# Performance work log

Measured on AMD Instinct MI355X. Metric: run time of the kernel, lower is better.

The kernel has to match this reference:

```python
import jax, jax.numpy as jnp
import numpy as np

N_AGT = 65536
N_CTX = 65536
E = 400000
D_AGT = 128
D_CTX = 128
EPS = 1e-5


def gn(x, w, b):
    # GroupNorm with num_groups=1 over channel dim of [N, C]
    m = jnp.mean(x, axis=-1, keepdims=True)
    v = jnp.mean((x - m) ** 2, axis=-1, keepdims=True)
    return (x - m) * jax.lax.rsqrt(v + EPS) * w + b


def setup_inputs() -> dict:
    key = jax.random.key(0)
    ks = jax.random.split(key, 24)
    s = 0.05
    inp = {
        "agts": jax.random.normal(ks[0], (N_AGT, D_AGT), jnp.float32),
        "ctx": jax.random.normal(ks[1], (N_CTX, D_CTX), jnp.float32),
        "agt_ctrs": jax.random.normal(ks[2], (N_AGT, 2), jnp.float32),
        "ctx_ctrs": jax.random.normal(ks[3], (N_CTX, 2), jnp.float32),
        "hi": jax.random.randint(ks[4], (E,), 0, N_AGT),
        "wi": jax.random.randint(ks[5], (E,), 0, N_CTX),
        # dist: Linear(2, n_ctx) + bias, ReLU, Linear(n_ctx, n_ctx) GN ng=1
        "dist_w1": jax.random.normal(ks[6], (2, D_CTX), jnp.float32) * s,
        "dist_b1": jnp.zeros((D_CTX,), jnp.float32),
        "dist_w2": jax.random.normal(ks[7], (D_CTX, D_CTX), jnp.float32) * s,
        "dist_gw": jnp.ones((D_CTX,), jnp.float32),
        "dist_gb": jnp.zeros((D_CTX,), jnp.float32),
        # query: Linear(n_agt, n_ctx) GN ng=1
        "q_w": jax.random.normal(ks[8], (D_AGT, D_CTX), jnp.float32) * s,
        "q_gw": jnp.ones((D_CTX,), jnp.float32),
        "q_gb": jnp.zeros((D_CTX,), jnp.float32),
        # ctx: Linear(3*n_ctx, n_agt) GN, then Linear(n_agt, n_agt, bias=False)
        "ctx_w1": jax.random.normal(ks[9], (3 * D_CTX, D_AGT), jnp.float32) * s,
        "ctx_gw": jnp.ones((D_AGT,), jnp.float32),
        "ctx_gb": jnp.zeros((D_AGT,), jnp.float32),
        "ctx_w2": jax.random.normal(ks[10], (D_AGT, D_AGT), jnp.float32) * s,
        # agt: Linear(n_agt, n_agt, bias=False)
        "agt_w": jax.random.normal(ks[11], (D_AGT, D_AGT), jnp.float32) * s,
        # norm: GroupNorm(1, n_agt)
        "norm_w": jnp.ones((D_AGT,), jnp.float32),
        "norm_b": jnp.zeros((D_AGT,), jnp.float32),
        # linear: Linear(n_agt, n_agt) GN, act=False
        "lin_w": jax.random.normal(ks[12], (D_AGT, D_AGT), jnp.float32) * s,
        "lin_gw": jnp.ones((D_AGT,), jnp.float32),
        "lin_gb": jnp.zeros((D_AGT,), jnp.float32),
    }
    return inp


def reference(agts, ctx, agt_ctrs, ctx_ctrs, hi, wi,
              dist_w1, dist_b1, dist_w2, dist_gw, dist_gb,
              q_w, q_gw, q_gb,
              ctx_w1, ctx_gw, ctx_gb, ctx_w2,
              agt_w, norm_w, norm_b,
              lin_w, lin_gw, lin_gb):
    res = agts
    # edge features: relative displacement -> dist MLP
    d = agt_ctrs[hi] - ctx_ctrs[wi]                      # [E, 2]
    d = jax.nn.relu(d @ dist_w1 + dist_b1)               # [E, D_CTX]
    d = jax.nn.relu(gn(d @ dist_w2, dist_gw, dist_gb))
    # query from gathered agent features
    q = jax.nn.relu(gn(agts[hi] @ q_w, q_gw, q_gb))      # [E, D_CTX]
    # gathered context features
    c = ctx[wi]                                          # [E, D_CTX]
    m = jnp.concatenate([d, q, c], axis=1)               # [E, 3*D_CTX]
    m = jax.nn.relu(gn(m @ ctx_w1, ctx_gw, ctx_gb))      # [E, D_AGT]
    m = m @ ctx_w2                                       # [E, D_AGT]
    # aggregate messages back to agents (scatter-add)
    out = agts @ agt_w
    out = out.at[hi].add(m)
    out = jax.nn.relu(gn(out, norm_w, norm_b))
    out = gn(out @ lin_w, lin_gw, lin_gb)                # act=False
    out = jax.nn.relu(out + res)
    return out
```

## Files before the change

kernel.cpp:

```cpp
#include <hip/hip_runtime.h>
#include <hip/hip_bf16.h>

#define TILE_E 32
#define WSTRIDE 132
#define SB 136
#define SF 132
#define FS 16384

#define FRAG_DW2 0
#define FRAG_W1D 1
#define FRAG_CW2 2
#define FRAG_AGT 3
#define FRAG_QW  4
#define FRAG_W1Q 5
#define FRAG_W1C 6
#define FRAG_LIN 7

typedef __attribute__((ext_vector_type(8))) short short8;
typedef __attribute__((ext_vector_type(4))) float f32x4;

__device__ __forceinline__ unsigned short f2bf(float f) {
    union { float f; unsigned u; } v; v.f = f;
    unsigned r = v.u + 0x7fff + ((v.u >> 16) & 1);
    return (unsigned short)(r >> 16);
}

__device__ __forceinline__ float bf2f(unsigned short u) {
    union { unsigned v; float f; } x; x.v = ((unsigned)u) << 16; return x.f;
}

__device__ __forceinline__ f32x4 mfma16(short8 a, short8 b, f32x4 c) {
    return __builtin_amdgcn_mfma_f32_16x16x32_bf16(a, b, c, 0, 0, 0);
}

__device__ __forceinline__ void load_bfrags_fast(const unsigned short* __restrict__ F,
                                                 int wv, int lane, short8 wB[2][4])
{
#pragma unroll
    for (int cb = 0; cb < 2; ++cb)
#pragma unroll
    for (int kc = 0; kc < 4; ++kc)
        wB[cb][kc] = *(const short8*)(F + ((((wv * 2 + cb) * 4 + kc) * 64 + lane) << 3));
}

__device__ __forceinline__ void mfma_gemm32(const unsigned short* __restrict__ X,
                                            const short8 wB[2][4],
                                            f32x4 acc[2][2], int lane)
{
    const int r  = lane & 15;
    const int kg = (lane >> 4) & 3;
#pragma unroll
    for (int rb = 0; rb < 2; ++rb) {
        const unsigned short* xp = X + (rb * 16 + r) * SB + kg * 8;
#pragma unroll
        for (int kc = 0; kc < 4; ++kc) {
            short8 a = *(const short8*)(xp + kc * 32);
            acc[rb][0] = mfma16(a, wB[0][kc], acc[rb][0]);
            acc[rb][1] = mfma16(a, wB[1][kc], acc[rb][1]);
        }
    }
}

__device__ __forceinline__ void gn_core_pack(float vals[16],
                                             const float* __restrict__ gw,
                                             const float* __restrict__ gb,
                                             int c0, short8& o0, short8& o1)
{
    float s1 = 0.f, s2 = 0.f;
#pragma unroll
    for (int i = 0; i < 16; ++i) { s1 += vals[i]; s2 += vals[i] * vals[i]; }
#pragma unroll
    for (int off = 4; off >= 1; off >>= 1) {
        s1 += __shfl_xor(s1, off);
        s2 += __shfl_xor(s2, off);
    }
    float m   = s1 * (1.f / 128.f);
    float var = fmaxf(s2 * (1.f / 128.f) - m * m, 0.f);
    float isc = rsqrtf(var + 1e-5f);
#pragma unroll
    for (int i = 0; i < 16; ++i) {
        float y = fmaxf((vals[i] - m) * isc * gw[c0 + i] + gb[c0 + i], 0.f);
        unsigned short u = f2bf(y);
        if (i < 8) o0[i] = (short)u; else o1[i - 8] = (short)u;
    }
}

__device__ __forceinline__ void gn_row_to_bf16(const float* __restrict__ sY,
                                               const float* __restrict__ gw,
                                               const float* __restrict__ gb,
                                               unsigned short* __restrict__ dst,
                                               int r8, int c0)
{
    const float4* yv = (const float4*)(sY + r8 * SF + c0);
    float4 a = yv[0], b = yv[1], c = yv[2], d = yv[3];
    float vals[16] = { a.x,a.y,a.z,a.w, b.x,b.y,b.z,b.w,
                       c.x,c.y,c.z,c.w, d.x,d.y,d.z,d.w };
    short8 o0, o1;
    gn_core_pack(vals, gw, gb, c0, o0, o1);
    short8* dp = (short8*)(dst + r8 * SB + c0);
    dp[0] = o0; dp[1] = o1;
}

__device__ __forceinline__ void gn_bf_to_bf16(const unsigned short* __restrict__ sYb,
                                              const float* __restrict__ gw,
                                              const float* __restrict__ gb,
                                              unsigned short* __restrict__ dst,
                                              int r8, int c0)
{
    const short8* yv = (const short8*)(sYb + r8 * SB + c0);
    short8 a = yv[0], b = yv[1];
    float vals[16];
#pragma unroll
    for (int i = 0; i < 8; ++i) {
        vals[i]     = bf2f((unsigned short)a[i]);
        vals[8 + i] = bf2f((unsigned short)b[i]);
    }
    short8 o0, o1;
    gn_core_pack(vals, gw, gb, c0, o0, o1);
    short8* dp = (short8*)(dst + r8 * SB + c0);
    dp[0] = o0; dp[1] = o1;
}

__global__ __launch_bounds__(256) void prep_hist_kernel(
    const float* __restrict__ W0, const float* __restrict__ W1,
    const float* __restrict__ W2, const float* __restrict__ W3,
    const float* __restrict__ W4, const float* __restrict__ W5,
    const float* __restrict__ W6, const float* __restrict__ W7,
    unsigned short* __restrict__ dst,
    const int* __restrict__ hi, int* __restrict__ hist, int E)
{
    const int b = blockIdx.x;
    if (b < 512) {
        int t = b * 256 + threadIdx.x;
        int m = t >> 14;
        int e = t & (FS - 1);
        int j    = e & 7;
        int lane = (e >> 3) & 63;
        int kc   = (e >> 9) & 3;
        int cb   = (e >> 11) & 1;
        int wv   = (e >> 12) & 3;
        int k = kc * 32 + ((lane >> 4) & 3) * 8 + j;
        int c = wv * 32 + cb * 16 + (lane & 15);
        const float* W = m == 0 ? W0 : m == 1 ? W1 : m == 2 ? W2 : m == 3 ? W3
                       : m == 4 ? W4 : m == 5 ? W5 : m == 6 ? W6 : W7;
        dst[t] = f2bf(W[k * 128 + c]);
    } else {
        for (int i = (b - 512) * 256 + threadIdx.x; i < E; i += 256 * 256)
            atomicAdd(&hist[hi[i]], 1);
    }
}

__global__ __launch_bounds__(256) void scanA_kernel(const int* __restrict__ hist,
                                                    int* __restrict__ csum, int nbins)
{
    __shared__ int red[4];
    int b = blockIdx.x;
    int idx = b * 256 + threadIdx.x;
    int v = (idx < nbins) ? hist[idx] : 0;
#pragma unroll
    for (int off = 32; off >= 1; off >>= 1) v += __shfl_xor(v, off);
    if ((threadIdx.x & 63) == 0) red[threadIdx.x >> 6] = v;
    __syncthreads();
    if (threadIdx.x == 0) csum[b] = red[0] + red[1] + red[2] + red[3];
}

__global__ __launch_bounds__(256) void scanBC_kernel(const int* __restrict__ hist,
                                                     const int* __restrict__ csum,
                                                     int* __restrict__ binCtr,
                                                     int nbins, int nchunks)
{
    __shared__ int part[256];
    __shared__ int red[4];
    __shared__ int coffb;
    const int b = blockIdx.x, t = threadIdx.x;

    int cv = (t < b && t < nchunks) ? csum[t] : 0;
#pragma unroll
    for (int off = 32; off >= 1; off >>= 1) cv += __shfl_xor(cv, off);
    if ((t & 63) == 0) red[t >> 6] = cv;
    __syncthreads();
    if (t == 0) coffb = red[0] + red[1] + red[2] + red[3];

    int idx = b * 256 + t;
    int v = (idx < nbins) ? hist[idx] : 0;
    part[t] = v;
    __syncthreads();
    for (int off = 1; off < 256; off <<= 1) {
        int p = (t >= off) ? part[t - off] : 0;
        __syncthreads();
        part[t] += p;
        __syncthreads();
    }
    if (idx < nbins) binCtr[idx] = part[t] - v + coffb;
}

__device__ __forceinline__ void kq_tile_body(
    int tile, const float* __restrict__ agts,
    const float* __restrict__ q_gw, const float* __restrict__ q_gb,
    const unsigned short* __restrict__ frags,
    float* __restrict__ qm, int N,
    unsigned short* sX, float* sY, float* sGw, float* sGb)
{
    const int tid  = threadIdx.x;
    const int lane = tid & 63;
    const int wv   = tid >> 6;
    const int colbase = wv * 32;
    const int r8 = tid >> 3, c0 = (tid & 7) * 16;
    const int cl = lane & 15, rq = lane >> 4;

    short8 wBq[2][4], wB1[2][4];
    load_bfrags_fast(frags + FRAG_QW  * FS, wv, lane, wBq);
    load_bfrags_fast(frags + FRAG_W1Q * FS, wv, lane, wB1);
    if (tid < 128) { sGw[tid] = q_gw[tid]; sGb[tid] = q_gb[tid]; }

    const int base = tile * 32;
    {
        int row = base + r8; if (row >= N) row = N - 1;
        const float* src = agts + (size_t)row * 128 + c0;
        short8 v0, v1;
#pragma unroll
        for (int i = 0; i < 8; ++i) { v0[i] = (short)f2bf(src[i]); v1[i] = (short)f2bf(src[i + 8]); }
        short8* dp = (short8*)(sX + r8 * SB + c0);
        dp[0] = v0; dp[1] = v1;
    }
    __syncthreads();

    f32x4 aQ[2][2] = {{{0,0,0,0},{0,0,0,0}},{{0,0,0,0},{0,0,0,0}}};
    mfma_gemm32(sX, wBq, aQ, lane);
    {
#pragma unroll
        for (int rb = 0; rb < 2; ++rb)
#pragma unroll
        for (int cb = 0; cb < 2; ++cb)
#pragma unroll
        for (int q = 0; q < 4; ++q)
            sY[(rb * 16 + rq * 4 + q) * SF + colbase + cb * 16 + cl] = aQ[rb][cb][q];
    }
    __syncthreads();
    gn_row_to_bf16(sY, sGw, sGb, sX, r8, c0);
    __syncthreads();

    f32x4 aM[2][2] = {{{0,0,0,0},{0,0,0,0}},{{0,0,0,0},{0,0,0,0}}};
    mfma_gemm32(sX, wB1, aM, lane);
#pragma unroll
    for (int rb = 0; rb < 2; ++rb)
#pragma unroll
    for (int q = 0; q < 4; ++q) {
        int row = base + rb * 16 + rq * 4 + q;
        if (row < N) {
            float2 v = make_float2(aM[rb][0][q], aM[rb][1][q]);
            *(float2*)(qm + (size_t)row * 128 + colbase + cl * 2) = v;
        }
    }
}

__device__ __forceinline__ void kc_tile_body(
    int tile, const float* __restrict__ ctx,
    const unsigned short* __restrict__ frags,
    float* __restrict__ cm, int N, unsigned short* sX)
{
    const int tid  = threadIdx.x;
    const int lane = tid & 63;
    const int wv   = tid >> 6;
    const int colbase = wv * 32;
    const int r8 = tid >> 3, c0 = (tid & 7) * 16;
    const int cl = lane & 15, rq = lane >> 4;

    short8 wB[2][4];
    load_bfrags_fast(frags + FRAG_W1C * FS, wv, lane, wB);

    const int base = tile * 32;
    {
        int row = base + r8; if (row >= N) row = N - 1;
        const float* src = ctx + (size_t)row * 128 + c0;
        short8 v0, v1;
#pragma unroll
        for (int i = 0; i < 8; ++i) { v0[i] = (short)f2bf(src[i]); v1[i] = (short)f2bf(src[i + 8]); }
        short8* dp = (short8*)(sX + r8 * SB + c0);
        dp[0] = v0; dp[1] = v1;
    }
    __syncthreads();

    f32x4 acc[2][2] = {{{0,0,0,0},{0,0,0,0}},{{0,0,0,0},{0,0,0,0}}};
    mfma_gemm32(sX, wB, acc, lane);
#pragma unroll
    for (int rb = 0; rb < 2; ++rb)
#pragma unroll
    for (int q = 0; q < 4; ++q) {
        int row = base + rb * 16 + rq * 4 + q;
        if (row < N) {
            float2 v = make_float2(acc[rb][0][q], acc[rb][1][q]);
            *(float2*)(cm + (size_t)row * 128 + colbase + cl * 2) = v;
        }
    }
}

__global__ __launch_bounds__(256) void nodes_kernel(
    const int* __restrict__ hi, const int* __restrict__ wi,
    const float* __restrict__ agt_ctrs, const float* __restrict__ ctx_ctrs,
    int* __restrict__ binCtr,
    int* __restrict__ hiS, int* __restrict__ wiS,
    float* __restrict__ dxS, float* __restrict__ dyS,
    const float* __restrict__ agts, const float* __restrict__ ctx,
    const float* __restrict__ q_gw, const float* __restrict__ q_gb,
    const unsigned short* __restrict__ frags,
    float* __restrict__ qm, float* __restrict__ cm,
    int E, int N, int NC, int tilesA)
{
    __shared__ __align__(16) unsigned short sX[32 * SB];
    __shared__ __align__(16) float sY[32 * SF];
    __shared__ float sGw[128], sGb[128];

    const int b = blockIdx.x;
    if (b < 256) {
        for (int i = b * 256 + threadIdx.x; i < E; i += 256 * 256) {
            int h = hi[i], w = wi[i];
            int p = atomicAdd(&binCtr[h], 1);
            hiS[p] = h; wiS[p] = w;
            dxS[p] = agt_ctrs[2 * h]     - ctx_ctrs[2 * w];
            dyS[p] = agt_ctrs[2 * h + 1] - ctx_ctrs[2 * w + 1];
        }
        return;
    }
    int t = b - 256;
    if (t < tilesA)
        kq_tile_body(t, agts, q_gw, q_gb, frags, qm, N, sX, sY, sGw, sGb);
    else
        kc_tile_body(t - tilesA, ctx, frags, cm, NC, sX);
}

__global__ __launch_bounds__(256, 3) void edge_sorted_kernel(
    const int* __restrict__ hiS, const int* __restrict__ wiS,
    const float* __restrict__ dxS, const float* __restrict__ dyS,
    const float* __restrict__ dist_w1, const float* __restrict__ dist_b1,
    const float* __restrict__ dist_gw, const float* __restrict__ dist_gb,
    const float* __restrict__ ctx_gw, const float* __restrict__ ctx_gb,
    const unsigned short* __restrict__ frags,
    const float* __restrict__ qm, const float* __restrict__ cm,
    float* __restrict__ msum, int E, int numTiles)
{
    __shared__ __align__(16) unsigned short sH[32 * SB];
    __shared__ __align__(16) unsigned short sYb[32 * SB];
    __shared__ float sW1[3][128];
    __shared__ float sDGw[128], sDGb[128], sCGw[128], sCGb[128];
    __shared__ int sHiA[32], sWiA[32], sKey[33];
    __shared__ float sDx[32], sDy[32];

    const int tid  = threadIdx.x;
    const int lane = tid & 63;
    const int wv   = tid >> 6;
    const int colbase = wv * 32;
    const int r8 = tid >> 3, c0 = (tid & 7) * 16;
    const int cl = lane & 15, rq = lane >> 4;

    short8 wBh[2][4], wBd[2][4];
    load_bfrags_fast(frags + FRAG_DW2 * FS, wv, lane, wBh);
    load_bfrags_fast(frags + FRAG_W1D * FS, wv, lane, wBd);
    if (tid < 128) {
        sW1[0][tid] = dist_w1[tid];
        sW1[1][tid] = dist_w1[128 + tid];
        sW1[2][tid] = dist_b1[tid];
        sDGw[tid] = dist_gw[tid]; sDGb[tid] = dist_gb[tid];
        sCGw[tid] = ctx_gw[tid];  sCGb[tid] = ctx_gb[tid];
    }

    int ph = 0, pw = 0, pkey = -1; float pdx = 0.f, pdy = 0.f;
    if (tid < 32) {
        pkey = -1 - tid;
        int e = blockIdx.x * 32 + tid;
        if (e < E) { ph = hiS[e]; pw = wiS[e]; pkey = ph; pdx = dxS[e]; pdy = dyS[e]; }
    }

    for (int tile = blockIdx.x; tile < numTiles; tile += gridDim.x) {
        __syncthreads();
        if (tid < 32) {
            sHiA[tid] = ph; sWiA[tid] = pw; sKey[tid] = pkey;
            sDx[tid] = pdx; sDy[tid] = pdy;
        }
        __syncthreads();

        if (tid < 32) {
            pkey = -1 - tid; ph = 0; pw = 0; pdx = 0.f; pdy = 0.f;
            int tn = tile + gridDim.x;
            if (tn < numTiles) {
                int e = tn * 32 + tid;
                if (e < E) { ph = hiS[e]; pw = wiS[e]; pkey = ph; pdx = dxS[e]; pdy = dyS[e]; }
            }
        }

        float2 gq[2][4], gc[2][4];
#pragma unroll
        for (int rb = 0; rb < 2; ++rb)
#pragma unroll
        for (int q = 0; q < 4; ++q) {
            int r = rb * 16 + rq * 4 + q;
            gq[rb][q] = *(const float2*)(qm + (size_t)sHiA[r] * 128 + colbase + cl * 2);
            gc[rb][q] = *(const float2*)(cm + (size_t)sWiA[r] * 128 + colbase + cl * 2);
        }

        {
            float dx = sDx[r8], dy = sDy[r8];
            short8 o0, o1;
#pragma unroll
            for (int i = 0; i < 16; ++i) {
                int c = c0 + i;
                float v = fmaf(dx, sW1[0][c], fmaf(dy, sW1[1][c], sW1[2][c]));
                unsigned short u = f2bf(fmaxf(v, 0.f));
                if (i < 8) o0[i] = (short)u; else o1[i - 8] = (short)u;
            }
            short8* dp = (short8*)(sH + r8 * SB + c0);
            dp[0] = o0; dp[1] = o1;
        }
        __syncthreads();

        f32x4 acc[2][2] = {{{0,0,0,0},{0,0,0,0}},{{0,0,0,0},{0,0,0,0}}};
        mfma_gemm32(sH, wBh, acc, lane);
        {
#pragma unroll
            for (int rb = 0; rb < 2; ++rb)
#pragma unroll
            for (int cb = 0; cb < 2; ++cb)
#pragma unroll
            for (int q = 0; q < 4; ++q)
                sYb[(rb * 16 + rq * 4 + q) * SB + colbase + cb * 16 + cl] = f2bf(acc[rb][cb][q]);
        }
        __syncthreads();
        gn_bf_to_bf16(sYb, sDGw, sDGb, sH, r8, c0);
        __syncthreads();

        f32x4 a2[2][2];
#pragma unroll
        for (int rb = 0; rb < 2; ++rb)
#pragma unroll
        for (int q = 0; q < 4; ++q) {
            a2[rb][0][q] = gq[rb][q].x + gc[rb][q].x;
            a2[rb][1][q] = gq[rb][q].y + gc[rb][q].y;
        }
        mfma_gemm32(sH, wBd, a2, lane);
        {
#pragma unroll
            for (int rb = 0; rb < 2; ++rb)
#pragma unroll
            for (int cb = 0; cb < 2; ++cb)
#pragma unroll
            for (int q = 0; q < 4; ++q)
                sYb[(rb * 16 + rq * 4 + q) * SB + colbase + cb * 16 + cl] = f2bf(a2[rb][cb][q]);
        }
        __syncthreads();
        gn_bf_to_bf16(sYb, sCGw, sCGb, sH, r8, c0);
        __syncthreads();

        {
            const int col   = tid & 127;
            const int rbase = (tid >> 7) * 16;
            float sum = 0.f;
#pragma unroll
            for (int i = 0; i < 16; ++i) {
                int r = rbase + i;
                sum += bf2f(sH[r * SB + col]);
                bool segEnd = (i == 15) || (sKey[r + 1] != sKey[r]);
                if (segEnd) {
                    int key = sKey[r];
                    if (key >= 0) atomicAdd(&msum[(size_t)key * 128 + col], sum);
                    sum = 0.f;
                }
            }
        }
    }
}

__global__ __launch_bounds__(256) void final_mfma_kernel(
    const float* __restrict__ agts, const float* __restrict__ msum,
    const float* __restrict__ norm_w, const float* __restrict__ norm_b,
    const float* __restrict__ lin_gw, const float* __restrict__ lin_gb,
    const unsigned short* __restrict__ frags,
    float* __restrict__ out, int N)
{
    __shared__ __align__(16) unsigned short sXa[32 * SB];
    __shared__ __align__(16) unsigned short sXm[32 * SB];
    __shared__ float sNw[128], sNb[128], sLw[128], sLb[128];

    const int tid  = threadIdx.x;
    const int lane = tid & 63;
    const int wv   = tid >> 6;
    const int colbase = wv * 32;
    const int r8 = tid >> 3, c0 = (tid & 7) * 16;
    const int cl = lane & 15, rq = lane >> 4;

    short8 wBa[2][4], wB2[2][4], wBl[2][4];
    load_bfrags_fast(frags + FRAG_AGT * FS, wv, lane, wBa);
    load_bfrags_fast(frags + FRAG_CW2 * FS, wv, lane, wB2);
    load_bfrags_fast(frags + FRAG_LIN * FS, wv, lane, wBl);
    if (tid < 128) {
        sNw[tid] = norm_w[tid]; sNb[tid] = norm_b[tid];
        sLw[tid] = lin_gw[tid]; sLb[tid] = lin_gb[tid];
    }

    const int base = blockIdx.x * 32;
    {
        int row = base + r8; if (row >= N) row = N - 1;
        const float* sa = agts + (size_t)row * 128 + c0;
        const float* sm = msum + (size_t)row * 128 + c0;
        short8 a0, a1, m0, m1;
#pragma unroll
        for (int i = 0; i < 8; ++i) {
            a0[i] = (short)f2bf(sa[i]); a1[i] = (short)f2bf(sa[i + 8]);
            m0[i] = (short)f2bf(sm[i]); m1[i] = (short)f2bf(sm[i + 8]);
        }
        short8* da = (short8*)(sXa + r8 * SB + c0);
        short8* dm = (short8*)(sXm + r8 * SB + c0);
        da[0] = a0; da[1] = a1; dm[0] = m0; dm[1] = m1;
    }
    __syncthreads();

    f32x4 acc[2][2] = {{{0,0,0,0},{0,0,0,0}},{{0,0,0,0},{0,0,0,0}}};
    mfma_gemm32(sXa, wBa, acc, lane);
    mfma_gemm32(sXm, wB2, acc, lane);
    __syncthreads();
    {
#pragma unroll
        for (int rb = 0; rb < 2; ++rb)
#pragma unroll
        for (int cb = 0; cb < 2; ++cb)
#pragma unroll
        for (int q = 0; q < 4; ++q)
            sXm[(rb * 16 + rq * 4 + q) * SB + colbase + cb * 16 + cl] = f2bf(acc[rb][cb][q]);
    }
    __syncthreads();
    gn_bf_to_bf16(sXm, sNw, sNb, sXa, r8, c0);
    __syncthreads();

    f32x4 aL[2][2] = {{{0,0,0,0},{0,0,0,0}},{{0,0,0,0},{0,0,0,0}}};
    mfma_gemm32(sXa, wBl, aL, lane);
    __syncthreads();
    {
#pragma unroll
        for (int rb = 0; rb < 2; ++rb)
#pragma unroll
        for (int cb = 0; cb < 2; ++cb)
#pragma unroll
        for (int q = 0; q < 4; ++q)
            sXm[(rb * 16 + rq * 4 + q) * SB + colbase + cb * 16 + cl] = f2bf(aL[rb][cb][q]);
    }
    __syncthreads();
    {
        int row = base + r8;
        if (row < N) {
            const short8* yv = (const short8*)(sXm + r8 * SB + c0);
            short8 a = yv[0], b = yv[1];
            float vals[16]; float s1 = 0.f, s2 = 0.f;
#pragma unroll
            for (int i = 0; i < 8; ++i) {
                vals[i]     = bf2f((unsigned short)a[i]);
                vals[8 + i] = bf2f((unsigned short)b[i]);
            }
#pragma unroll
            for (int i = 0; i < 16; ++i) { s1 += vals[i]; s2 += vals[i] * vals[i]; }
#pragma unroll
            for (int off = 4; off >= 1; off >>= 1) {
                s1 += __shfl_xor(s1, off);
                s2 += __shfl_xor(s2, off);
            }
            float m   = s1 * (1.f / 128.f);
            float var = fmaxf(s2 * (1.f / 128.f) - m * m, 0.f);
            float isc = rsqrtf(var + 1e-5f);
            const float* rp = agts + (size_t)row * 128 + c0;
            float* op = out + (size_t)row * 128 + c0;
#pragma unroll
            for (int i = 0; i < 16; ++i) {
                float y = (vals[i] - m) * isc * sLw[c0 + i] + sLb[c0 + i] + rp[i];
                op[i] = fmaxf(y, 0.f);
            }
        }
    }
}

__device__ __forceinline__ void gemm_tile(const float* __restrict__ sX,
                                          const float* __restrict__ sWT,
                                          int lc, int rg,
                                          float acc0[8], float acc1[8])
{
    const float* w0p = sWT + lc * WSTRIDE;
    const float* w1p = sWT + (lc + 64) * WSTRIDE;
    const float* xp  = sX + rg * 8 * WSTRIDE;
#pragma unroll 4
    for (int k = 0; k < 128; k += 4) {
        float4 w0 = *(const float4*)(w0p + k);
        float4 w1 = *(const float4*)(w1p + k);
#pragma unroll
        for (int j = 0; j < 8; ++j) {
            float4 x = *(const float4*)(xp + j * WSTRIDE + k);
            acc0[j] = fmaf(x.x, w0.x, acc0[j]);
            acc0[j] = fmaf(x.y, w0.y, acc0[j]);
            acc0[j] = fmaf(x.z, w0.z, acc0[j]);
            acc0[j] = fmaf(x.w, w0.w, acc0[j]);
            acc1[j] = fmaf(x.x, w1.x, acc1[j]);
            acc1[j] = fmaf(x.y, w1.y, acc1[j]);
            acc1[j] = fmaf(x.z, w1.z, acc1[j]);
            acc1[j] = fmaf(x.w, w1.w, acc1[j]);
        }
    }
}

__device__ __forceinline__ void stage_wt(const float* __restrict__ W,
                                         float* __restrict__ sWT, int tid)
{
    const int c  = tid & 127;
    const int k0 = tid >> 7;
    float*       dst = sWT + c * WSTRIDE + k0;
    const float* src = W + tid;
    float v[16];
#pragma unroll
    for (int p = 0; p < 4; ++p) {
#pragma unroll
        for (int i = 0; i < 16; ++i) v[i] = src[(p * 16 + i) * 256];
#pragma unroll
        for (int i = 0; i < 16; ++i) dst[(p * 16 + i) * 2] = v[i];
    }
}

__device__ __forceinline__ void gn_rows_lds(const float acc0[8], const float acc1[8],
                                            float gw0, float gw1, float gb0, float gb1,
                                            bool relu, float* __restrict__ dst,
                                            int lc, int rg)
{
#pragma unroll
    for (int j = 0; j < 8; ++j) {
        float s1 = acc0[j] + acc1[j];
        float s2 = acc0[j] * acc0[j] + acc1[j] * acc1[j];
#pragma unroll
        for (int off = 32; off >= 1; off >>= 1) {
            s1 += __shfl_xor(s1, off);
            s2 += __shfl_xor(s2, off);
        }
        float m   = s1 * (1.f / 128.f);
        float var = fmaxf(s2 * (1.f / 128.f) - m * m, 0.f);
        float isc = rsqrtf(var + 1e-5f);
        float y0  = (acc0[j] - m) * isc * gw0 + gb0;
        float y1  = (acc1[j] - m) * isc * gw1 + gb1;
        if (relu) { y0 = fmaxf(y0, 0.f); y1 = fmaxf(y1, 0.f); }
        int r = rg * 8 + j;
        dst[r * WSTRIDE + lc]      = y0;
        dst[r * WSTRIDE + lc + 64] = y1;
    }
}

__global__ __launch_bounds__(256) void rowgemm_kernel(
    const float* __restrict__ X, const float* __restrict__ W,
    float* __restrict__ Y, int n)
{
    __shared__ float sWT[128 * WSTRIDE];
    __shared__ float sX[TILE_E * WSTRIDE];
    const int tid  = threadIdx.x;
    const int base = blockIdx.x * TILE_E;
    {
        int r = tid >> 3, c0 = (tid & 7) * 16;
        int row = base + r;
        if (row < n) {
            const float* src = X + (size_t)row * 128 + c0;
            float*       dst = sX + r * WSTRIDE + c0;
#pragma unroll
            for (int i = 0; i < 4; ++i)
                *(float4*)(dst + i * 4) = *(const float4*)(src + i * 4);
        }
    }
    stage_wt(W, sWT, tid);
    __syncthreads();
    const int lc = tid & 63, rg = tid >> 6;
    float acc0[8] = {0,0,0,0,0,0,0,0}, acc1[8] = {0,0,0,0,0,0,0,0};
    gemm_tile(sX, sWT, lc, rg, acc0, acc1);
#pragma unroll
    for (int j = 0; j < 8; ++j) {
        int row = base + rg * 8 + j;
        if (row < n) {
            Y[(size_t)row * 128 + lc]      = acc0[j];
            Y[(size_t)row * 128 + lc + 64] = acc1[j];
        }
    }
}

__global__ __launch_bounds__(256) void edge_kernel(
    const float* __restrict__ agt_ctrs, const float* __restrict__ ctx_ctrs,
    const int* __restrict__ hi, const int* __restrict__ wi,
    const float* __restrict__ qsrc, const float* __restrict__ ctx,
    const float* __restrict__ dist_w1, const float* __restrict__ dist_b1,
    const float* __restrict__ dist_w2,
    const float* __restrict__ dist_gw, const float* __restrict__ dist_gb,
    const float* __restrict__ q_w,
    const float* __restrict__ q_gw, const float* __restrict__ q_gb,
    const float* __restrict__ ctx_w1,
    const float* __restrict__ ctx_gw, const float* __restrict__ ctx_gb,
    const float* __restrict__ ctx_w2,
    float* __restrict__ out, int E, int numTiles)
{
    __shared__ float sWT[128 * WSTRIDE];
    __shared__ float sH2[TILE_E * WSTRIDE];
    __shared__ float sD2[TILE_E * WSTRIDE];
    __shared__ float sQ2[TILE_E * WSTRIDE];
    __shared__ float sC2[TILE_E * WSTRIDE];
    __shared__ int   sHi[TILE_E];
    __shared__ int   sWiB[TILE_E];
    __shared__ float sDx2[TILE_E], sDy2[TILE_E];

    const int tid = threadIdx.x;
    const int lc = tid & 63, rg = tid >> 6;

    const float dgw0 = dist_gw[lc], dgw1 = dist_gw[lc + 64];
    const float dgb0 = dist_gb[lc], dgb1 = dist_gb[lc + 64];
    const float cgw0 = ctx_gw[lc],  cgw1 = ctx_gw[lc + 64];
    const float cgb0 = ctx_gb[lc],  cgb1 = ctx_gb[lc + 64];
    const float qgw0 = q_gw[lc], qgw1 = q_gw[lc + 64];
    const float qgb0 = q_gb[lc], qgb1 = q_gb[lc + 64];
    const int   hc  = tid & 127;
    const int   hrg = tid >> 7;
    const float w1x = dist_w1[hc], w1y = dist_w1[128 + hc], b1c = dist_b1[hc];

    for (int tile = blockIdx.x; tile < numTiles; tile += gridDim.x) {
        const int base = tile * TILE_E;
        __syncthreads();
        if (tid < TILE_E) {
            int e = base + tid;
            int h = 0, w = 0;
            if (e < E) { h = hi[e]; w = wi[e]; }
            sHi[tid]  = h;
            sWiB[tid] = w;
            sDx2[tid] = agt_ctrs[2 * h]     - ctx_ctrs[2 * w];
            sDy2[tid] = agt_ctrs[2 * h + 1] - ctx_ctrs[2 * w + 1];
        }
        __syncthreads();
        {
            int r = tid >> 3, c0 = (tid & 7) * 16;
            int h = sHi[r], w = sWiB[r];
            const float* qs = qsrc + (size_t)h * 128 + c0;
            const float* cs = ctx  + (size_t)w * 128 + c0;
            float* qd = sQ2 + r * WSTRIDE + c0;
            float* cd = sC2 + r * WSTRIDE + c0;
#pragma unroll
            for (int i = 0; i < 4; ++i) {
                *(float4*)(qd + i * 4) = *(const float4*)(qs + i * 4);
                *(float4*)(cd + i * 4) = *(const float4*)(cs + i * 4);
            }
        }
        {
#pragma unroll
            for (int j = 0; j < 16; ++j) {
                int r = hrg * 16 + j;
                float v = fmaf(sDx2[r], w1x, fmaf(sDy2[r], w1y, b1c));
                sH2[r * WSTRIDE + hc] = fmaxf(v, 0.f);
            }
        }
        __syncthreads();
        stage_wt(q_w, sWT, tid);
        __syncthreads();
        {
            float a0[8] = {0,0,0,0,0,0,0,0}, a1[8] = {0,0,0,0,0,0,0,0};
            gemm_tile(sQ2, sWT, lc, rg, a0, a1);
            __syncthreads();
            gn_rows_lds(a0, a1, qgw0, qgw1, qgb0, qgb1, true, sQ2, lc, rg);
        }
        __syncthreads();
        stage_wt(dist_w2, sWT, tid);
        __syncthreads();
        {
            float a0[8] = {0,0,0,0,0,0,0,0}, a1[8] = {0,0,0,0,0,0,0,0};
            gemm_tile(sH2, sWT, lc, rg, a0, a1);
            gn_rows_lds(a0, a1, dgw0, dgw1, dgb0, dgb1, true, sD2, lc, rg);
        }
        float m0[8] = {0,0,0,0,0,0,0,0}, m1[8] = {0,0,0,0,0,0,0,0};
        __syncthreads();
        stage_wt(ctx_w1, sWT, tid);
        __syncthreads();
        gemm_tile(sD2, sWT, lc, rg, m0, m1);
        __syncthreads();
        stage_wt(ctx_w1 + 128 * 128, sWT, tid);
        __syncthreads();
        gemm_tile(sQ2, sWT, lc, rg, m0, m1);
        __syncthreads();
        stage_wt(ctx_w1 + 2 * 128 * 128, sWT, tid);
        __syncthreads();
        gemm_tile(sC2, sWT, lc, rg, m0, m1);
        gn_rows_lds(m0, m1, cgw0, cgw1, cgb0, cgb1, true, sH2, lc, rg);
        __syncthreads();
        stage_wt(ctx_w2, sWT, tid);
        __syncthreads();
        {
            float a0[8] = {0,0,0,0,0,0,0,0}, a1[8] = {0,0,0,0,0,0,0,0};
            gemm_tile(sH2, sWT, lc, rg, a0, a1);
#pragma unroll
            for (int j = 0; j < 8; ++j) {
                int r = rg * 8 + j;
                int e = base + r;
                if (e < E) {
                    int h = sHi[r];
                    atomicAdd(&out[(size_t)h * 128 + lc],      a0[j]);
                    atomicAdd(&out[(size_t)h * 128 + lc + 64], a1[j]);
                }
            }
        }
    }
}

__global__ __launch_bounds__(256) void final_kernel(
    const float* __restrict__ agts,
    const float* __restrict__ norm_w, const float* __restrict__ norm_b,
    const float* __restrict__ lin_w,
    const float* __restrict__ lin_gw, const float* __restrict__ lin_gb,
    float* __restrict__ out, int n)
{
    __shared__ float sWT[128 * WSTRIDE];
    __shared__ float sX[TILE_E * WSTRIDE];
    const int tid  = threadIdx.x;
    const int base = blockIdx.x * TILE_E;
    {
        int r = tid >> 3, c0 = (tid & 7) * 16;
        int row = base + r;
        if (row < n) {
            const float* src = out + (size_t)row * 128 + c0;
            float vals[16];
            float s1 = 0.f, s2 = 0.f;
#pragma unroll
            for (int i = 0; i < 16; ++i) {
                float v = src[i];
                vals[i] = v; s1 += v; s2 += v * v;
            }
#pragma unroll
            for (int off = 4; off >= 1; off >>= 1) {
                s1 += __shfl_xor(s1, off);
                s2 += __shfl_xor(s2, off);
            }
            float m   = s1 * (1.f / 128.f);
            float var = fmaxf(s2 * (1.f / 128.f) - m * m, 0.f);
            float isc = rsqrtf(var + 1e-5f);
            float* dst = sX + r * WSTRIDE + c0;
#pragma unroll
            for (int i = 0; i < 16; ++i) {
                int c = c0 + i;
                float y = (vals[i] - m) * isc * norm_w[c] + norm_b[c];
                dst[i] = fmaxf(y, 0.f);
            }
        }
    }
    stage_wt(lin_w, sWT, tid);
    __syncthreads();
    const int lc = tid & 63, rg = tid >> 6;
    float acc0[8] = {0,0,0,0,0,0,0,0}, acc1[8] = {0,0,0,0,0,0,0,0};
    gemm_tile(sX, sWT, lc, rg, acc0, acc1);
    const float lgw0 = lin_gw[lc], lgw1 = lin_gw[lc + 64];
    const float lgb0 = lin_gb[lc], lgb1 = lin_gb[lc + 64];
#pragma unroll
    for (int j = 0; j < 8; ++j) {
        float s1 = acc0[j] + acc1[j];
        float s2 = acc0[j] * acc0[j] + acc1[j] * acc1[j];
#pragma unroll
        for (int off = 32; off >= 1; off >>= 1) {
            s1 += __shfl_xor(s1, off);
            s2 += __shfl_xor(s2, off);
        }
        float m   = s1 * (1.f / 128.f);
        float var = fmaxf(s2 * (1.f / 128.f) - m * m, 0.f);
        float isc = rsqrtf(var + 1e-5f);
        int row = base + rg * 8 + j;
        if (row < n) {
            size_t ro = (size_t)row * 128;
            float y0 = (acc0[j] - m) * isc * lgw0 + lgb0 + agts[ro + lc];
            float y1 = (acc1[j] - m) * isc * lgw1 + lgb1 + agts[ro + lc + 64];
            out[ro + lc]      = fmaxf(y0, 0.f);
            out[ro + lc + 64] = fmaxf(y1, 0.f);
        }
    }
}

extern "C" void kernel_launch(void* const* d_in, const int* in_sizes, int n_in,
                              void* d_out, int out_size, void* d_ws, size_t ws_size,
                              hipStream_t stream)
{
    const float* agts     = (const float*)d_in[0];
    const float* ctx      = (const float*)d_in[1];
    const float* agt_ctrs = (const float*)d_in[2];
    const float* ctx_ctrs = (const float*)d_in[3];
    const int*   hi       = (const int*)d_in[4];
    const int*   wi       = (const int*)d_in[5];
    const float* dist_w1  = (const float*)d_in[6];
    const float* dist_b1  = (const float*)d_in[7];
    const float* dist_w2  = (const float*)d_in[8];
    const float* dist_gw  = (const float*)d_in[9];
    const float* dist_gb  = (const float*)d_in[10];
    const float* q_w      = (const float*)d_in[11];
    const float* q_gw     = (const float*)d_in[12];
    const float* q_gb     = (const float*)d_in[13];
    const float* ctx_w1   = (const float*)d_in[14];
    const float* ctx_gw   = (const float*)d_in[15];
    const float* ctx_gb   = (const float*)d_in[16];
    const float* ctx_w2   = (const float*)d_in[17];
    const float* agt_w    = (const float*)d_in[18];
    const float* norm_w   = (const float*)d_in[19];
    const float* norm_b   = (const float*)d_in[20];
    const float* lin_w    = (const float*)d_in[21];
    const float* lin_gw   = (const float*)d_in[22];
    const float* lin_gb   = (const float*)d_in[23];

    const int N  = in_sizes[0] / 128;
    const int NC = in_sizes[1] / 128;
    const int E  = in_sizes[4];
    float* out = (float*)d_out;

    const int tilesA   = (N + 31) / 32;
    const int tilesC   = (NC + 31) / 32;
    const int numTiles = (E + 31) / 32;
    const int nchunks  = (N + 255) / 256;

    const size_t needQM = (size_t)N  * 128 * sizeof(float);
    const size_t needCM = (size_t)NC * 128 * sizeof(float);
    const size_t needMS = (size_t)N  * 128 * sizeof(float);
    const size_t needH  = (size_t)N * sizeof(int);
    const size_t needB  = (size_t)N * sizeof(int);
    const size_t needE4 = (size_t)E * sizeof(int);
    const size_t needF  = (size_t)8 * FS * sizeof(unsigned short);
    const size_t needSc = 512 * sizeof(int);
    const size_t needTotal = needQM + needCM + needMS + needH + needB
                           + 4 * needE4 + needF + needSc;

    if (ws_size >= needTotal && nchunks <= 256) {
        char* w = (char*)d_ws;
        float*          qm     = (float*)w;            w += needQM;
        float*          cm     = (float*)w;            w += needCM;
        float*          msum   = (float*)w;            w += needMS;
        int*            hist   = (int*)w;              w += needH;
        int*            binCtr = (int*)w;              w += needB;
        int*            hiS    = (int*)w;              w += needE4;
        int*            wiS    = (int*)w;              w += needE4;
        float*          dxS    = (float*)w;            w += needE4;
        float*          dyS    = (float*)w;            w += needE4;
        int*            csum   = (int*)w;              w += 512 * sizeof(int);
        unsigned short* fragsW = (unsigned short*)w;   w += needF;

        hipMemsetAsync(msum, 0, needMS + needH, stream);

        prep_hist_kernel<<<768, 256, 0, stream>>>(
            dist_w2, ctx_w1, ctx_w2, agt_w, q_w,
            ctx_w1 + 128 * 128, ctx_w1 + 2 * 128 * 128, lin_w, fragsW,
            hi, hist, E);

        scanA_kernel<<<nchunks, 256, 0, stream>>>(hist, csum, N);
        scanBC_kernel<<<nchunks, 256, 0, stream>>>(hist, csum, binCtr, N, nchunks);

        nodes_kernel<<<256 + tilesA + tilesC, 256, 0, stream>>>(
            hi, wi, agt_ctrs, ctx_ctrs, binCtr, hiS, wiS, dxS, dyS,
            agts, ctx, q_gw, q_gb, fragsW, qm, cm,
            E, N, NC, tilesA);

        int gridE = numTiles < 2048 ? numTiles : 2048;
        edge_sorted_kernel<<<gridE, 256, 0, stream>>>(
            hiS, wiS, dxS, dyS,
            dist_w1, dist_b1, dist_gw, dist_gb, ctx_gw, ctx_gb,
            fragsW, qm, cm, msum, E, numTiles);

        final_mfma_kernel<<<tilesA, 256, 0, stream>>>(
            agts, msum, norm_w, norm_b, lin_gw, lin_gb, fragsW, out, N);
    } else {
        rowgemm_kernel<<<tilesA, 256, 0, stream>>>(agts, agt_w, out, N);
        int gridE = numTiles < 8192 ? numTiles : 8192;
        edge_kernel<<<gridE, 256, 0, stream>>>(agt_ctrs, ctx_ctrs, hi, wi,
            agts, ctx,
            dist_w1, dist_b1, dist_w2, dist_gw, dist_gb,
            q_w, q_gw, q_gb,
            ctx_w1, ctx_gw, ctx_gb, ctx_w2,
            out, E, numTiles);
        final_kernel<<<tilesA, 256, 0, stream>>>(agts, norm_w, norm_b,
            lin_w, lin_gw, lin_gb, out, N);
    }
}
```

Before: 219.5 us.

## Double edge tile to 64 rows and defer q/c gathers past first GEMM

The edge kernel now handles 64 edges per tile instead of 32, doubling the MFMA work per synchronisation and per load of the resident weight fragments. The grid is capped at 768 persistent blocks. The qm/cm gathers move to after the first GEMM, so they can overlap the GroupNorm pass instead of staying live across it, and the accumulators grow to 4x2 tiles. The bf16 conversion now uses the HIP intrinsic. Costs are higher register pressure and double the shared memory per block, which may reduce occupancy under launch_bounds(256,3), and longer serial segment-sum loops in the scatter stage.

```diff
diff --git a/kernel.cpp b/kernel.cpp
--- a/kernel.cpp
+++ b/kernel.cpp
@@ -20,9 +20,9 @@
 typedef __attribute__((ext_vector_type(4))) float f32x4;
 
 __device__ __forceinline__ unsigned short f2bf(float f) {
-    union { float f; unsigned u; } v; v.f = f;
-    unsigned r = v.u + 0x7fff + ((v.u >> 16) & 1);
-    return (unsigned short)(r >> 16);
+    __hip_bfloat16 h = __float2bfloat16(f);
+    unsigned short u; __builtin_memcpy(&u, &h, 2);
+    return u;
 }
 
 __device__ __forceinline__ float bf2f(unsigned short u) {
@@ -51,6 +51,24 @@
     const int kg = (lane >> 4) & 3;
 #pragma unroll
     for (int rb = 0; rb < 2; ++rb) {
+        const unsigned short* xp = X + (rb * 16 + r) * SB + kg * 8;
+#pragma unroll
+        for (int kc = 0; kc < 4; ++kc) {
+            short8 a = *(const short8*)(xp + kc * 32);
+            acc[rb][0] = mfma16(a, wB[0][kc], acc[rb][0]);
+            acc[rb][1] = mfma16(a, wB[1][kc], acc[rb][1]);
+        }
+    }
+}
+
+__device__ __forceinline__ void mfma_gemm64(const unsigned short* __restrict__ X,
+                                            const short8 wB[2][4],
+                                            f32x4 acc[4][2], int lane)
+{
+    const int r  = lane & 15;
+    const int kg = (lane >> 4) & 3;
+#pragma unroll
+    for (int rb = 0; rb < 4; ++rb) {
         const unsigned short* xp = X + (rb * 16 + r) * SB + kg * 8;
 #pragma unroll
         for (int kc = 0; kc < 4; ++kc) {
@@ -339,12 +357,12 @@
     const float* __restrict__ qm, const float* __restrict__ cm,
     float* __restrict__ msum, int E, int numTiles)
 {
-    __shared__ __align__(16) unsigned short sH[32 * SB];
-    __shared__ __align__(16) unsigned short sYb[32 * SB];
+    __shared__ __align__(16) unsigned short sH[64 * SB];
+    __shared__ __align__(16) unsigned short sYb[64 * SB];
     __shared__ float sW1[3][128];
     __shared__ float sDGw[128], sDGb[128], sCGw[128], sCGb[128];
-    __shared__ int sHiA[32], sWiA[32], sKey[33];
-    __shared__ float sDx[32], sDy[32];
+    __shared__ int sHiA[64], sWiA[64], sKey[65];
+    __shared__ float sDx[64], sDy[64];
 
     const int tid  = threadIdx.x;
     const int lane = tid & 63;
@@ -365,81 +383,83 @@
     }
 
     int ph = 0, pw = 0, pkey = -1; float pdx = 0.f, pdy = 0.f;
-    if (tid < 32) {
+    if (tid < 64) {
         pkey = -1 - tid;
-        int e = blockIdx.x * 32 + tid;
+        int e = blockIdx.x * 64 + tid;
         if (e < E) { ph = hiS[e]; pw = wiS[e]; pkey = ph; pdx = dxS[e]; pdy = dyS[e]; }
     }
 
     for (int tile = blockIdx.x; tile < numTiles; tile += gridDim.x) {
         __syncthreads();
-        if (tid < 32) {
+        if (tid < 64) {
             sHiA[tid] = ph; sWiA[tid] = pw; sKey[tid] = pkey;
             sDx[tid] = pdx; sDy[tid] = pdy;
         }
         __syncthreads();
 
-        if (tid < 32) {
+        if (tid < 64) {
             pkey = -1 - tid; ph = 0; pw = 0; pdx = 0.f; pdy = 0.f;
             int tn = tile + gridDim.x;
             if (tn < numTiles) {
-                int e = tn * 32 + tid;
+                int e = tn * 64 + tid;
                 if (e < E) { ph = hiS[e]; pw = wiS[e]; pkey = ph; pdx = dxS[e]; pdy = dyS[e]; }
             }
         }
 
-        float2 gq[2][4], gc[2][4];
-#pragma unroll
-        for (int rb = 0; rb < 2; ++rb)
+        {
+#pragma unroll
+            for (int p = 0; p < 2; ++p) {
+                int row = p * 32 + r8;
+                float dx = sDx[row], dy = sDy[row];
+                short8 o0, o1;
+#pragma unroll
+                for (int i = 0; i < 16; ++i) {
+                    int c = c0 + i;
+                    float v = fmaf(dx, sW1[0][c], fmaf(dy, sW1[1][c], sW1[2][c]));
+                    unsigned short u = f2bf(fmaxf(v, 0.f));
+                    if (i < 8) o0[i] = (short)u; else o1[i - 8] = (short)u;
+                }
+                short8* dp = (short8*)(sH + row * SB + c0);
+                dp[0] = o0; dp[1] = o1;
+            }
+        }
+        __syncthreads();
+
+        {
+            f32x4 acc[4][2] = {{{0,0,0,0},{0,0,0,0}},{{0,0,0,0},{0,0,0,0}},
+                               {{0,0,0,0},{0,0,0,0}},{{0,0,0,0},{0,0,0,0}}};
+            mfma_gemm64(sH, wBh, acc, lane);
+#pragma unroll
+            for (int rb = 0; rb < 4; ++rb)
+#pragma unroll
+            for (int cb = 0; cb < 2; ++cb)
+#pragma unroll
+            for (int q = 0; q < 4; ++q)
+                sYb[(rb * 16 + rq * 4 + q) * SB + colbase + cb * 16 + cl] = f2bf(acc[rb][cb][q]);
+        }
+        __syncthreads();
+
+        f32x4 a2[4][2];
+#pragma unroll
+        for (int rb = 0; rb < 4; ++rb)
 #pragma unroll
         for (int q = 0; q < 4; ++q) {
             int r = rb * 16 + rq * 4 + q;
-            gq[rb][q] = *(const float2*)(qm + (size_t)sHiA[r] * 128 + colbase + cl * 2);
-            gc[rb][q] = *(const float2*)(cm + (size_t)sWiA[r] * 128 + colbase + cl * 2);
-        }
-
+            float2 g1 = *(const float2*)(qm + (size_t)sHiA[r] * 128 + colbase + cl * 2);
+            float2 g2 = *(const float2*)(cm + (size_t)sWiA[r] * 128 + colbase + cl * 2);
+            a2[rb][0][q] = g1.x + g2.x;
+            a2[rb][1][q] = g1.y + g2.y;
+        }
+
+#pragma unroll
+        for (int p = 0; p < 2; ++p)
+            gn_bf_to_bf16(sYb, sDGw, sDGb, sH, p * 32 + r8, c0);
+        __syncthreads();
+
+        mfma_gemm64(sH, wBd, a2, lane);
         {
-            float dx = sDx[r8], dy = sDy[r8];
-            short8 o0, o1;
-#pragma unroll
-            for (int i = 0; i < 16; ++i) {
-                int c = c0 + i;
-                float v = fmaf(dx, sW1[0][c], fmaf(dy, sW1[1][c], sW1[2][c]));
-                unsigned short u = f2bf(fmaxf(v, 0.f));
-                if (i < 8) o0[i] = (short)u; else o1[i - 8] = (short)u;
-            }
-            short8* dp = (short8*)(sH + r8 * SB + c0);
-            dp[0] = o0; dp[1] = o1;
-        }
-        __syncthreads();
-
-        f32x4 acc[2][2] = {{{0,0,0,0},{0,0,0,0}},{{0,0,0,0},{0,0,0,0}}};
-        mfma_gemm32(sH, wBh, acc, lane);
-        {
-#pragma unroll
-            for (int rb = 0; rb < 2; ++rb)
-#pragma unroll
-            for (int cb = 0; cb < 2; ++cb)
-#pragma unroll
-            for (int q = 0; q < 4; ++q)
-                sYb[(rb * 16 + rq * 4 + q) * SB + colbase + cb * 16 + cl] = f2bf(acc[rb][cb][q]);
-        }
-        __syncthreads();
-        gn_bf_to_bf16(sYb, sDGw, sDGb, sH, r8, c0);
-        __syncthreads();
-
-        f32x4 a2[2][2];
-#pragma unroll
-        for (int rb = 0; rb < 2; ++rb)
-#pragma unroll
-        for (int q = 0; q < 4; ++q) {
-            a2[rb][0][q] = gq[rb][q].x + gc[rb][q].x;
-            a2[rb][1][q] = gq[rb][q].y + gc[rb][q].y;
-        }
-        mfma_gemm32(sH, wBd, a2, lane);
-        {
-#pragma unroll
-            for (int rb = 0; rb < 2; ++rb)
+#pragma unroll
+            for (int rb = 0; rb < 4; ++rb)
 #pragma unroll
             for (int cb = 0; cb < 2; ++cb)
 #pragma unroll
@@ -447,18 +467,20 @@
                 sYb[(rb * 16 + rq * 4 + q) * SB + colbase + cb * 16 + cl] = f2bf(a2[rb][cb][q]);
         }
         __syncthreads();
-        gn_bf_to_bf16(sYb, sCGw, sCGb, sH, r8, c0);
+#pragma unroll
+        for (int p = 0; p < 2; ++p)
+            gn_bf_to_bf16(sYb, sCGw, sCGb, sH, p * 32 + r8, c0);
         __syncthreads();
 
         {
             const int col   = tid & 127;
-            const int rbase = (tid >> 7) * 16;
+            const int rbase = (tid >> 7) * 32;
             float sum = 0.f;
 #pragma unroll
-            for (int i = 0; i < 16; ++i) {
+            for (int i = 0; i < 32; ++i) {
                 int r = rbase + i;
                 sum += bf2f(sH[r * SB + col]);
-                bool segEnd = (i == 15) || (sKey[r + 1] != sKey[r]);
+                bool segEnd = (i == 31) || (sKey[r + 1] != sKey[r]);
                 if (segEnd) {
                     int key = sKey[r];
                     if (key >= 0) atomicAdd(&msum[(size_t)key * 128 + col], sum);
@@ -907,6 +929,7 @@
     const int tilesA   = (N + 31) / 32;
     const int tilesC   = (NC + 31) / 32;
     const int numTiles = (E + 31) / 32;
+    const int numT64   = (E + 63) / 64;
     const int nchunks  = (N + 255) / 256;
 
     const size_t needQM = (size_t)N  * 128 * sizeof(float);
@@ -949,11 +972,11 @@
             agts, ctx, q_gw, q_gb, fragsW, qm, cm,
             E, N, NC, tilesA);
 
-        int gridE = numTiles < 2048 ? numTiles : 2048;
+        int gridE = numT64 < 768 ? numT64 : 768;
         edge_sorted_kernel<<<gridE, 256, 0, stream>>>(
             hiS, wiS, dxS, dyS,
             dist_w1, dist_b1, dist_gw, dist_gb, ctx_gw, ctx_gb,
-            fragsW, qm, cm, msum, E, numTiles);
+            fragsW, qm, cm, msum, E, numT64);
 
         final_mfma_kernel<<<tilesA, 256, 0, stream>>>(
             agts, msum, norm_w, norm_b, lin_gw, lin_gb, fragsW, out, N);
```

Result: slower. 277.6 us (+26.5%).
